# Kernel optimization log

Hardware: AMD Instinct MI355X
Metric: run time of the kernel (lower is better)

The kernel has to match this reference:

```python
import jax, jax.numpy as jnp
import numpy as np

B, S, D_MODEL = 1, 2048, 2048
H, KVH = 16, 4
HD = D_MODEL // H          # 128
N_REP = H // KVH           # 4 (GQA)
WINDOW = 1024              # window_size=(WINDOW-1, 0): self + 1023 past tokens
CLIP = 8.0
THETA = 500000.0
EPS = 1e-6
SCALE = 1.0 / (HD ** 0.5)


def rms_norm(x, w):
    # per-head RMSNorm over last dim (head_dim)
    var = jnp.mean(jnp.square(x), axis=-1, keepdims=True)
    return x * jax.lax.rsqrt(var + EPS) * w


def rope_tables():
    inv_freq = 1.0 / (THETA ** (jnp.arange(0, HD, 2, dtype=jnp.float32) / HD))
    pos = jnp.arange(S, dtype=jnp.float32)
    freqs = pos[:, None] * inv_freq[None, :]          # [S, HD/2]
    emb = jnp.concatenate([freqs, freqs], axis=-1)    # [S, HD]
    return jnp.cos(emb), jnp.sin(emb)


def rotate_half(x):
    x1, x2 = x[..., : HD // 2], x[..., HD // 2 :]
    return jnp.concatenate([-x2, x1], axis=-1)


def apply_rope(x, cos, sin):
    # x: [B, S, h, HD]; cos/sin: [S, HD]
    return x * cos[None, :, None, :] + rotate_half(x) * sin[None, :, None, :]


def setup_inputs() -> dict:
    key = jax.random.key(0)
    ks = jax.random.split(key, 7)
    w = lambda k, shape: jax.random.normal(k, shape, jnp.float32) * 0.02
    return {
        "x": jax.random.normal(ks[0], (B, S, D_MODEL), jnp.float32),
        "w_q": w(ks[1], (D_MODEL, D_MODEL)),
        "w_k": w(ks[2], (KVH * HD, D_MODEL)),
        "w_v": w(ks[3], (KVH * HD, D_MODEL)),
        "w_out": w(ks[4], (D_MODEL, D_MODEL)),
        "q_norm_w": jnp.ones((HD,), jnp.float32),
        "k_norm_w": jnp.ones((HD,), jnp.float32),
        "sinks": jax.random.normal(ks[5], (H,), jnp.float32),
    }


def reference(x, w_q, w_k, w_v, w_out, q_norm_w, k_norm_w, sinks):
    # fused QKV projection + clip
    q = jnp.clip(x @ w_q.T, -CLIP, CLIP).reshape(B, S, H, HD)
    k = jnp.clip(x @ w_k.T, -CLIP, CLIP).reshape(B, S, KVH, HD)
    v = jnp.clip(x @ w_v.T, -CLIP, CLIP).reshape(B, S, KVH, HD)

    # per-head qk RMSNorm, then RoPE
    q = rms_norm(q, q_norm_w)
    k = rms_norm(k, k_norm_w)
    cos, sin = rope_tables()
    q = apply_rope(q, cos, sin)
    k = apply_rope(k, cos, sin)

    # GQA: repeat_interleave kv heads
    k = jnp.repeat(k, N_REP, axis=2)  # [B, S, H, HD]
    v = jnp.repeat(v, N_REP, axis=2)

    # sliding-window causal attention with a learned per-head sink logit
    logits = jnp.einsum("bqhd,bkhd->bhqk", q, k) * SCALE  # [B, H, S, S]
    qi = jnp.arange(S)[:, None]
    ki = jnp.arange(S)[None, :]
    mask = (ki <= qi) & (ki > qi - WINDOW)                # causal + window
    logits = jnp.where(mask[None, None, :, :], logits, -jnp.inf)

    # sink token: always-visible extra logit sinks[h] with zero value vector
    sink_col = jnp.broadcast_to(sinks[None, :, None, None], (B, H, S, 1))
    full = jnp.concatenate([logits, sink_col], axis=-1)   # [B, H, S, S+1]
    probs = jax.nn.softmax(full, axis=-1)

    att = jnp.einsum("bhqk,bkhd->bqhd", probs[..., :S], v)  # sink value is 0
    return att.reshape(B, S, D_MODEL) @ w_out.T
```

## Files before the change

### kernel.cpp

```cpp
#include <hip/hip_runtime.h>
#include <hip/hip_bf16.h>
#include <math.h>

#define S_LEN 2048
#define DMODEL 2048
#define NH 16
#define NKVH 4
#define HDIM 128
#define WINDOW 1024

typedef __bf16 bf16;
typedef __bf16 bf16x8 __attribute__((ext_vector_type(8)));
typedef __bf16 bf16x4 __attribute__((ext_vector_type(4)));
typedef float floatx4 __attribute__((ext_vector_type(4)));

static __device__ __forceinline__ bf16x8 load_bf8(const bf16* p) {
    return *reinterpret_cast<const bf16x8*>(p);
}

static __device__ __forceinline__ void async16(const bf16* g, bf16* l) {
    __builtin_amdgcn_global_load_lds(
        (const __attribute__((address_space(1))) void*)g,
        (__attribute__((address_space(3))) void*)l, 16, 0, 0);
}

__global__ __launch_bounds__(256) void convert_kernel(
    const float* __restrict__ x, const float* __restrict__ wq,
    const float* __restrict__ wk, const float* __restrict__ wv,
    const float* __restrict__ wo,
    bf16* __restrict__ xb, bf16* __restrict__ wqb, bf16* __restrict__ wkb,
    bf16* __restrict__ wvb, bf16* __restrict__ wob) {
    for (int i = blockIdx.x * blockDim.x + threadIdx.x; i < 3670016;
         i += gridDim.x * blockDim.x) {
        const float* src; bf16* dst; int off;
        if      (i < 1048576) { src = x;  dst = xb;  off = i; }
        else if (i < 2097152) { src = wq; dst = wqb; off = i - 1048576; }
        else if (i < 2359296) { src = wk; dst = wkb; off = i - 2097152; }
        else if (i < 2621440) { src = wv; dst = wvb; off = i - 2359296; }
        else                  { src = wo; dst = wob; off = i - 2621440; }
        float4 v = reinterpret_cast<const float4*>(src)[off];
        union { bf16 b[4]; ushort4 u; } t;
        t.b[0] = (bf16)v.x; t.b[1] = (bf16)v.y;
        t.b[2] = (bf16)v.z; t.b[3] = (bf16)v.w;
        reinterpret_cast<ushort4*>(dst)[off] = t.u;
    }
}

__global__ __launch_bounds__(256, 1) void gemm_qkv_fused(
    const bf16* __restrict__ A, const bf16* __restrict__ B,
    const float* __restrict__ qw, const float* __restrict__ kw,
    bf16* __restrict__ qb, bf16* __restrict__ kb, bf16* __restrict__ vtb) {
    const int K = 2048;
    int flat = blockIdx.x;
    int xcd = flat & 7, w = flat >> 3;
    int mrow = xcd * 2 + (w >= 12);
    int ncol = (w >= 12) ? (w - 12) : w;
    int m0 = mrow * 128, n0 = ncol * 256;
    __shared__ __align__(16) bf16 smem[3 * 24576];
    int tid = threadIdx.x;
    int lane = tid & 63, wid = tid >> 6;
    int l15 = lane & 15, quad = lane >> 4;
    int rlocal = lane >> 3;
    int scol = ((lane & 7) ^ rlocal) * 8;
    const bf16* gA = A + (size_t)(m0 + wid * 32 + rlocal) * K + scol;
    const bf16* gB = B + (size_t)(n0 + wid * 64 + rlocal) * K + scol;
    int mb = (wid & 1) * 64, nb = (wid >> 1) * 128;

    floatx4 acc[4][8];
#pragma unroll
    for (int mi = 0; mi < 4; ++mi)
#pragma unroll
        for (int ni = 0; ni < 8; ++ni) acc[mi][ni] = floatx4{0.f, 0.f, 0.f, 0.f};

#pragma unroll
    for (int s = 0; s < 2; ++s) {
        bf16* dst = smem + s * 24576;
#pragma unroll
        for (int j = 0; j < 4; ++j)
            async16(gA + (size_t)(j * 8) * K + s * 64,
                    dst + (wid * 32 + j * 8) * 64);
#pragma unroll
        for (int j = 0; j < 8; ++j)
            async16(gB + (size_t)(j * 8) * K + s * 64,
                    dst + 8192 + (wid * 64 + j * 8) * 64);
    }

    int slot = 0;
#pragma unroll 1
    for (int t = 0; t < 32; ++t) {
        if (t < 31) asm volatile("s_waitcnt vmcnt(12)" ::: "memory");
        else        asm volatile("s_waitcnt vmcnt(0)" ::: "memory");
        __builtin_amdgcn_s_barrier();
        __builtin_amdgcn_sched_barrier(0);
        if (t < 30) {
            int s2 = slot + 2; if (s2 >= 3) s2 -= 3;
            bf16* dst = smem + s2 * 24576;
            int kof = (t + 2) * 64;
#pragma unroll
            for (int j = 0; j < 4; ++j)
                async16(gA + (size_t)(j * 8) * K + kof,
                        dst + (wid * 32 + j * 8) * 64);
#pragma unroll
            for (int j = 0; j < 8; ++j)
                async16(gB + (size_t)(j * 8) * K + kof,
                        dst + 8192 + (wid * 64 + j * 8) * 64);
        }
        const bf16* sA = smem + slot * 24576;
        const bf16* sB = sA + 8192;
#pragma unroll
        for (int kc = 0; kc < 2; ++kc) {
            bf16x8 af[4], bq[8];
            int ch = ((kc << 2) + quad) ^ (l15 & 7);
#pragma unroll
            for (int i = 0; i < 4; ++i)
                af[i] = load_bf8(sA + (mb + i * 16 + l15) * 64 + ch * 8);
#pragma unroll
            for (int n = 0; n < 8; ++n)
                bq[n] = load_bf8(sB + (nb + n * 16 + l15) * 64 + ch * 8);
#pragma unroll
            for (int mi = 0; mi < 4; ++mi)
#pragma unroll
                for (int ni = 0; ni < 8; ++ni)
                    acc[mi][ni] = __builtin_amdgcn_mfma_f32_16x16x32_bf16(
                        af[mi], bq[ni], acc[mi][ni], 0, 0, 0);
        }
        ++slot; if (slot == 3) slot = 0;
    }

#pragma unroll
    for (int mi = 0; mi < 4; ++mi)
#pragma unroll
        for (int ni = 0; ni < 8; ++ni)
#pragma unroll
            for (int r = 0; r < 4; ++r)
                acc[mi][ni][r] = fminf(fmaxf(acc[mi][ni][r], -8.0f), 8.0f);

    if (n0 >= 2560) {
#pragma unroll
        for (int mi = 0; mi < 4; ++mi)
#pragma unroll
            for (int ni = 0; ni < 8; ++ni)
#pragma unroll
                for (int r = 0; r < 4; ++r) {
                    int row = m0 + mb + mi * 16 + quad * 4 + r;
                    int n = n0 + nb + ni * 16 + l15;
                    vtb[(size_t)(n - 2560) * 2048 + row] = (bf16)acc[mi][ni][r];
                }
        return;
    }

    const float* nw = (n0 < 2048) ? qw : kw;
    float nwv[8];
#pragma unroll
    for (int ni = 0; ni < 8; ++ni) nwv[ni] = nw[(nb + ni * 16 + l15) & 127];
#pragma unroll
    for (int mi = 0; mi < 4; ++mi)
#pragma unroll
        for (int r = 0; r < 4; ++r) {
            float s = 0.f;
#pragma unroll
            for (int ni = 0; ni < 8; ++ni) s += acc[mi][ni][r] * acc[mi][ni][r];
#pragma unroll
            for (int o = 1; o < 16; o <<= 1) s += __shfl_xor(s, o, 64);
            float rinv = rsqrtf(s * (1.0f / 128.0f) + 1e-6f);
#pragma unroll
            for (int ni = 0; ni < 8; ++ni) acc[mi][ni][r] *= rinv * nwv[ni];
        }

    float invf[4];
#pragma unroll
    for (int ni = 0; ni < 4; ++ni) {
        int fi = ni * 16 + l15;
        invf[ni] = __expf((float)fi * (-13.122363377404328f / 64.0f));
    }
#pragma unroll
    for (int mi = 0; mi < 4; ++mi)
#pragma unroll
        for (int r = 0; r < 4; ++r) {
            int row = mb + mi * 16 + quad * 4 + r;
            int s = m0 + row;
            float pos = (float)s;
#pragma unroll
            for (int ni = 0; ni < 4; ++ni) {
                float ang = pos * invf[ni];
                float c = __cosf(ang), sn = __sinf(ang);
                float a = acc[mi][ni][r], b2 = acc[mi][ni + 4][r];
                float olo = a * c - b2 * sn;
                float ohi = b2 * c + a * sn;
                int nlo = n0 + nb + ni * 16 + l15;
                if (n0 < 2048) {
                    qb[(size_t)s * 2048 + nlo] = (bf16)olo;
                    qb[(size_t)s * 2048 + nlo + 64] = (bf16)ohi;
                } else {
                    kb[(size_t)s * 512 + (nlo - 2048)] = (bf16)olo;
                    kb[(size_t)s * 512 + (nlo - 2048) + 64] = (bf16)ohi;
                }
            }
        }
}

__global__ __launch_bounds__(256, 1) void gemm_out(
    const bf16* __restrict__ A, const bf16* __restrict__ B,
    float* __restrict__ C) {
    const int K = 2048, N = 2048;
    int flat = blockIdx.x;
    int xcd = flat & 7, w = flat >> 3;
    int m0 = (xcd * 2 + (w >> 4)) * 128;
    int n0 = (w & 15) * 128;
    __shared__ __align__(16) bf16 smem[3 * 16384];
    int tid = threadIdx.x;
    int lane = tid & 63, wid = tid >> 6;
    int l15 = lane & 15, quad = lane >> 4;
    int rlocal = lane >> 3;
    int scol = ((lane & 7) ^ rlocal) * 8;
    const bf16* gA = A + (size_t)(m0 + wid * 32 + rlocal) * K + scol;
    const bf16* gB = B + (size_t)(n0 + wid * 32 + rlocal) * K + scol;
    int mb = (wid & 1) * 64, nb = (wid >> 1) * 64;

    floatx4 acc[4][4];
#pragma unroll
    for (int mi = 0; mi < 4; ++mi)
#pragma unroll
        for (int ni = 0; ni < 4; ++ni) acc[mi][ni] = floatx4{0.f, 0.f, 0.f, 0.f};

#pragma unroll
    for (int s = 0; s < 2; ++s) {
        bf16* dst = smem + s * 16384;
#pragma unroll
        for (int j = 0; j < 4; ++j) {
            async16(gA + (size_t)(j * 8) * K + s * 64,
                    dst + (wid * 32 + j * 8) * 64);
            async16(gB + (size_t)(j * 8) * K + s * 64,
                    dst + 8192 + (wid * 32 + j * 8) * 64);
        }
    }

    int slot = 0;
#pragma unroll 1
    for (int t = 0; t < 32; ++t) {
        if (t < 31) asm volatile("s_waitcnt vmcnt(8)" ::: "memory");
        else        asm volatile("s_waitcnt vmcnt(0)" ::: "memory");
        __builtin_amdgcn_s_barrier();
        __builtin_amdgcn_sched_barrier(0);
        if (t < 30) {
            int s2 = slot + 2; if (s2 >= 3) s2 -= 3;
            bf16* dst = smem + s2 * 16384;
            int kof = (t + 2) * 64;
#pragma unroll
            for (int j = 0; j < 4; ++j) {
                async16(gA + (size_t)(j * 8) * K + kof,
                        dst + (wid * 32 + j * 8) * 64);
                async16(gB + (size_t)(j * 8) * K + kof,
                        dst + 8192 + (wid * 32 + j * 8) * 64);
            }
        }
        const bf16* sA = smem + slot * 16384;
        const bf16* sB = sA + 8192;
#pragma unroll
        for (int kc = 0; kc < 2; ++kc) {
            bf16x8 af[4], bq[4];
            int ch = ((kc << 2) + quad) ^ (l15 & 7);
#pragma unroll
            for (int i = 0; i < 4; ++i)
                af[i] = load_bf8(sA + (mb + i * 16 + l15) * 64 + ch * 8);
#pragma unroll
            for (int n = 0; n < 4; ++n)
                bq[n] = load_bf8(sB + (nb + n * 16 + l15) * 64 + ch * 8);
#pragma unroll
            for (int mi = 0; mi < 4; ++mi)
#pragma unroll
                for (int ni = 0; ni < 4; ++ni)
                    acc[mi][ni] = __builtin_amdgcn_mfma_f32_16x16x32_bf16(
                        af[mi], bq[ni], acc[mi][ni], 0, 0, 0);
        }
        ++slot; if (slot == 3) slot = 0;
    }

#pragma unroll
    for (int mi = 0; mi < 4; ++mi)
#pragma unroll
        for (int ni = 0; ni < 4; ++ni)
#pragma unroll
            for (int r = 0; r < 4; ++r) {
                int m = m0 + mb + mi * 16 + quad * 4 + r;
                int n = n0 + nb + ni * 16 + l15;
                C[(size_t)m * N + n] = acc[mi][ni][r];
            }
}

__global__ __launch_bounds__(256) void attn(
    const bf16* __restrict__ qb, const bf16* __restrict__ kb,
    const bf16* __restrict__ vtb, const float* __restrict__ sinks,
    bf16* __restrict__ attb) {
    __shared__ __align__(16) bf16 sK[2][64 * 128];
    __shared__ __align__(16) bf16 sV[2][128 * 64];
    __shared__ __align__(16) bf16 sP[64 * 72];
    __shared__ float redu[64][4];
    int tid = threadIdx.x;
    int lane = tid & 63, wid = tid >> 6;
    int l15 = lane & 15, quad = lane >> 4;
    int flat = blockIdx.x;
    int xcd = flat & 7, w = flat >> 3;
    int h = xcd * 2 + (w >> 5);
    int kh = h >> 2;
    int bq0 = (w & 31) * 64;

    bf16x8 qf[4][4];
#pragma unroll
    for (int ni = 0; ni < 4; ++ni) {
        const bf16* qrow = qb + (size_t)(bq0 + ni * 16 + l15) * 2048 + h * 128 + quad * 8;
#pragma unroll
        for (int kc = 0; kc < 4; ++kc) qf[ni][kc] = load_bf8(qrow + kc * 32);
    }

    floatx4 acc[4][2];
#pragma unroll
    for (int mi = 0; mi < 4; ++mi)
#pragma unroll
        for (int df = 0; df < 2; ++df) acc[mi][df] = floatx4{0.f, 0.f, 0.f, 0.f};
    float lpq[4];
#pragma unroll
    for (int ni = 0; ni < 4; ++ni) lpq[ni] = 0.f;

    int keyit = wid * 4 + (lane >> 4);
    int gcK = (lane & 15) ^ keyit;
    int dimit = wid * 8 + (lane >> 3);
    int gcV = (lane & 7) ^ ((lane >> 3) & 7);

    int tstart = bq0 - 1024; if (tstart < 0) tstart = 0;
    const bf16* kbase = kb + (size_t)kh * 128;
    const bf16* vbase = vtb + (size_t)kh * 128 * 2048;

#pragma unroll
    for (int r = 0; r < 4; ++r) {
        async16(kbase + (size_t)(tstart + r * 16 + keyit) * 512 + gcK * 8,
                sK[0] + (r * 16 + wid * 4) * 128);
        async16(vbase + (size_t)(r * 32 + dimit) * 2048 + tstart + gcV * 8,
                sV[0] + (r * 32 + wid * 8) * 64);
    }

    int buf = 0;
    for (int t = tstart; t <= bq0; t += 64) {
        __syncthreads();
        if (t + 64 <= bq0) {
#pragma unroll
            for (int r = 0; r < 4; ++r) {
                async16(kbase + (size_t)(t + 64 + r * 16 + keyit) * 512 + gcK * 8,
                        sK[buf ^ 1] + (r * 16 + wid * 4) * 128);
                async16(vbase + (size_t)(r * 32 + dimit) * 2048 + t + 64 + gcV * 8,
                        sV[buf ^ 1] + (r * 32 + wid * 8) * 64);
            }
        }
        floatx4 ST[4];
#pragma unroll
        for (int ni = 0; ni < 4; ++ni) ST[ni] = floatx4{0.f, 0.f, 0.f, 0.f};
#pragma unroll
        for (int kc = 0; kc < 4; ++kc) {
            int ch = (kc * 4 + quad) ^ l15;
            bf16x8 kf = load_bf8(sK[buf] + (wid * 16 + l15) * 128 + ch * 8);
#pragma unroll
            for (int ni = 0; ni < 4; ++ni)
                ST[ni] = __builtin_amdgcn_mfma_f32_16x16x32_bf16(kf, qf[ni][kc], ST[ni], 0, 0, 0);
        }
        int kbi = t + wid * 16 + quad * 4;
#pragma unroll
        for (int ni = 0; ni < 4; ++ni) {
            int qi = bq0 + ni * 16 + l15;
            bf16x4 pv;
#pragma unroll
            for (int r = 0; r < 4; ++r) {
                int ki = kbi + r;
                float v = ST[ni][r] * 0.08838834764831845f;
                bool ok = (ki <= qi) && (ki > qi - WINDOW);
                float e = ok ? __expf(v) : 0.0f;
                lpq[ni] += e;
                pv[r] = (bf16)e;
            }
            *(bf16x4*)(sP + (ni * 16 + l15) * 72 + wid * 16 + quad * 4) = pv;
        }
        __syncthreads();
#pragma unroll
        for (int kc = 0; kc < 2; ++kc) {
            bf16x8 pf[4];
#pragma unroll
            for (int mi = 0; mi < 4; ++mi)
                pf[mi] = load_bf8(sP + (mi * 16 + l15) * 72 + kc * 32 + quad * 8);
#pragma unroll
            for (int df = 0; df < 2; ++df) {
                int dim = wid * 32 + df * 16 + l15;
                int ch = (kc * 4 + quad) ^ (l15 & 7);
                bf16x8 vf = load_bf8(sV[buf] + dim * 64 + ch * 8);
#pragma unroll
                for (int mi = 0; mi < 4; ++mi)
                    acc[mi][df] = __builtin_amdgcn_mfma_f32_16x16x32_bf16(pf[mi], vf, acc[mi][df], 0, 0, 0);
            }
        }
        buf ^= 1;
    }

#pragma unroll
    for (int ni = 0; ni < 4; ++ni) {
        float v = lpq[ni];
        v += __shfl_xor(v, 16, 64);
        v += __shfl_xor(v, 32, 64);
        if (quad == 0) redu[ni * 16 + l15][wid] = v;
    }
    __syncthreads();
    float sk = __expf(sinks[h]);
#pragma unroll
    for (int mi = 0; mi < 4; ++mi)
#pragma unroll
        for (int r = 0; r < 4; ++r) {
            int row = mi * 16 + quad * 4 + r;
            float rs = redu[row][0] + redu[row][1] + redu[row][2] + redu[row][3] + sk;
            float inv = 1.0f / rs;
#pragma unroll
            for (int df = 0; df < 2; ++df) {
                int dim = wid * 32 + df * 16 + l15;
                attb[(size_t)(bq0 + row) * 2048 + h * 128 + dim] =
                    (bf16)(acc[mi][df][r] * inv);
            }
        }
}

extern "C" void kernel_launch(void* const* d_in, const int* in_sizes, int n_in,
                              void* d_out, int out_size, void* d_ws, size_t ws_size,
                              hipStream_t stream) {
    const float* x      = (const float*)d_in[0];
    const float* w_q    = (const float*)d_in[1];
    const float* w_k    = (const float*)d_in[2];
    const float* w_v    = (const float*)d_in[3];
    const float* w_out  = (const float*)d_in[4];
    const float* q_norm = (const float*)d_in[5];
    const float* k_norm = (const float*)d_in[6];
    const float* sinks  = (const float*)d_in[7];

    char* ws = (char*)d_ws;
    const size_t MB = 1u << 20;
    bf16* xb   = (bf16*)(ws + 0 * MB);
    bf16* wqb  = (bf16*)(ws + 8 * MB);
    bf16* wkb  = (bf16*)(ws + 16 * MB);
    bf16* wvb  = (bf16*)(ws + 18 * MB);
    bf16* wob  = (bf16*)(ws + 20 * MB);
    bf16* qb   = (bf16*)(ws + 28 * MB);
    bf16* kb   = (bf16*)(ws + 36 * MB);
    bf16* vtb  = (bf16*)(ws + 38 * MB);
    bf16* attb = (bf16*)(ws + 40 * MB);
    bf16* wcomb = wqb;
    float* out = (float*)d_out;

    convert_kernel<<<2048, 256, 0, stream>>>(x, w_q, w_k, w_v, w_out,
                                             xb, wqb, wkb, wvb, wob);
    gemm_qkv_fused<<<192, 256, 0, stream>>>(xb, wcomb, q_norm, k_norm,
                                            qb, kb, vtb);
    attn<<<512, 256, 0, stream>>>(qb, kb, vtb, sinks, attb);
    gemm_out<<<256, 256, 0, stream>>>(attb, wob, out);
}
```

Before: 205.1 us.

## Process 128 queries per attention block with 8 waves sharing K/V tiles

The attention kernel now uses 512-thread blocks that each cover 128 query rows (two 64-row halves), so every K/V tile staged in LDS serves twice as many queries. Staging is split so waves 0-3 load K and waves 4-7 load V, and the key loop runs one extra tile to cover the second query half. The intent is to halve global K/V traffic per query and the async loads per wave. In exchange the grid drops from 512 to 256 blocks, the XCD-aware block-to-head mapping is removed, and the first query half does useless masked work on its last tile.

```diff
diff --git a/kernel.cpp b/kernel.cpp
--- a/kernel.cpp
+++ b/kernel.cpp
@@ -288,27 +288,27 @@
             }
 }
 
-__global__ __launch_bounds__(256) void attn(
+__global__ __launch_bounds__(512) void attn(
     const bf16* __restrict__ qb, const bf16* __restrict__ kb,
     const bf16* __restrict__ vtb, const float* __restrict__ sinks,
     bf16* __restrict__ attb) {
     __shared__ __align__(16) bf16 sK[2][64 * 128];
     __shared__ __align__(16) bf16 sV[2][128 * 64];
-    __shared__ __align__(16) bf16 sP[64 * 72];
-    __shared__ float redu[64][4];
+    __shared__ __align__(16) bf16 sP[128 * 72];
+    __shared__ float redu[128][4];
     int tid = threadIdx.x;
     int lane = tid & 63, wid = tid >> 6;
     int l15 = lane & 15, quad = lane >> 4;
-    int flat = blockIdx.x;
-    int xcd = flat & 7, w = flat >> 3;
-    int h = xcd * 2 + (w >> 5);
-    int kh = h >> 2;
-    int bq0 = (w & 31) * 64;
+    int kq = wid >> 1;
+    int qh = wid & 1;
+    int h = blockIdx.y, kh = h >> 2;
+    int bq0 = blockIdx.x * 128;
 
     bf16x8 qf[4][4];
 #pragma unroll
     for (int ni = 0; ni < 4; ++ni) {
-        const bf16* qrow = qb + (size_t)(bq0 + ni * 16 + l15) * 2048 + h * 128 + quad * 8;
+        const bf16* qrow = qb + (size_t)(bq0 + qh * 64 + ni * 16 + l15) * 2048
+                           + h * 128 + quad * 8;
 #pragma unroll
         for (int kc = 0; kc < 4; ++kc) qf[ni][kc] = load_bf8(qrow + kc * 32);
     }
@@ -322,33 +322,44 @@
 #pragma unroll
     for (int ni = 0; ni < 4; ++ni) lpq[ni] = 0.f;
 
-    int keyit = wid * 4 + (lane >> 4);
+    int sw = wid & 3;
+    int keyit = sw * 4 + (lane >> 4);
     int gcK = (lane & 15) ^ keyit;
-    int dimit = wid * 8 + (lane >> 3);
+    int dimit = sw * 8 + (lane >> 3);
     int gcV = (lane & 7) ^ ((lane >> 3) & 7);
+    bool stageK = (wid < 4);
 
     int tstart = bq0 - 1024; if (tstart < 0) tstart = 0;
+    int tEnd = bq0 + 64;
     const bf16* kbase = kb + (size_t)kh * 128;
     const bf16* vbase = vtb + (size_t)kh * 128 * 2048;
 
-#pragma unroll
-    for (int r = 0; r < 4; ++r) {
-        async16(kbase + (size_t)(tstart + r * 16 + keyit) * 512 + gcK * 8,
-                sK[0] + (r * 16 + wid * 4) * 128);
-        async16(vbase + (size_t)(r * 32 + dimit) * 2048 + tstart + gcV * 8,
-                sV[0] + (r * 32 + wid * 8) * 64);
+    if (stageK) {
+#pragma unroll
+        for (int r = 0; r < 4; ++r)
+            async16(kbase + (size_t)(tstart + r * 16 + keyit) * 512 + gcK * 8,
+                    sK[0] + (r * 16 + sw * 4) * 128);
+    } else {
+#pragma unroll
+        for (int r = 0; r < 4; ++r)
+            async16(vbase + (size_t)(r * 32 + dimit) * 2048 + tstart + gcV * 8,
+                    sV[0] + (r * 32 + sw * 8) * 64);
     }
 
     int buf = 0;
-    for (int t = tstart; t <= bq0; t += 64) {
+    for (int t = tstart; t <= tEnd; t += 64) {
         __syncthreads();
-        if (t + 64 <= bq0) {
-#pragma unroll
-            for (int r = 0; r < 4; ++r) {
-                async16(kbase + (size_t)(t + 64 + r * 16 + keyit) * 512 + gcK * 8,
-                        sK[buf ^ 1] + (r * 16 + wid * 4) * 128);
-                async16(vbase + (size_t)(r * 32 + dimit) * 2048 + t + 64 + gcV * 8,
-                        sV[buf ^ 1] + (r * 32 + wid * 8) * 64);
+        if (t + 64 <= tEnd) {
+            if (stageK) {
+#pragma unroll
+                for (int r = 0; r < 4; ++r)
+                    async16(kbase + (size_t)(t + 64 + r * 16 + keyit) * 512 + gcK * 8,
+                            sK[buf ^ 1] + (r * 16 + sw * 4) * 128);
+            } else {
+#pragma unroll
+                for (int r = 0; r < 4; ++r)
+                    async16(vbase + (size_t)(r * 32 + dimit) * 2048 + t + 64 + gcV * 8,
+                            sV[buf ^ 1] + (r * 32 + sw * 8) * 64);
             }
         }
         floatx4 ST[4];
@@ -357,15 +368,15 @@
 #pragma unroll
         for (int kc = 0; kc < 4; ++kc) {
             int ch = (kc * 4 + quad) ^ l15;
-            bf16x8 kf = load_bf8(sK[buf] + (wid * 16 + l15) * 128 + ch * 8);
+            bf16x8 kf = load_bf8(sK[buf] + (kq * 16 + l15) * 128 + ch * 8);
 #pragma unroll
             for (int ni = 0; ni < 4; ++ni)
                 ST[ni] = __builtin_amdgcn_mfma_f32_16x16x32_bf16(kf, qf[ni][kc], ST[ni], 0, 0, 0);
         }
-        int kbi = t + wid * 16 + quad * 4;
+        int kbi = t + kq * 16 + quad * 4;
 #pragma unroll
         for (int ni = 0; ni < 4; ++ni) {
-            int qi = bq0 + ni * 16 + l15;
+            int qi = bq0 + qh * 64 + ni * 16 + l15;
             bf16x4 pv;
 #pragma unroll
             for (int r = 0; r < 4; ++r) {
@@ -376,7 +387,7 @@
                 lpq[ni] += e;
                 pv[r] = (bf16)e;
             }
-            *(bf16x4*)(sP + (ni * 16 + l15) * 72 + wid * 16 + quad * 4) = pv;
+            *(bf16x4*)(sP + (qh * 64 + ni * 16 + l15) * 72 + kq * 16 + quad * 4) = pv;
         }
         __syncthreads();
 #pragma unroll
@@ -384,10 +395,10 @@
             bf16x8 pf[4];
 #pragma unroll
             for (int mi = 0; mi < 4; ++mi)
-                pf[mi] = load_bf8(sP + (mi * 16 + l15) * 72 + kc * 32 + quad * 8);
+                pf[mi] = load_bf8(sP + (qh * 64 + mi * 16 + l15) * 72 + kc * 32 + quad * 8);
 #pragma unroll
             for (int df = 0; df < 2; ++df) {
-                int dim = wid * 32 + df * 16 + l15;
+                int dim = kq * 32 + df * 16 + l15;
                 int ch = (kc * 4 + quad) ^ (l15 & 7);
                 bf16x8 vf = load_bf8(sV[buf] + dim * 64 + ch * 8);
 #pragma unroll
@@ -403,7 +414,7 @@
         float v = lpq[ni];
         v += __shfl_xor(v, 16, 64);
         v += __shfl_xor(v, 32, 64);
-        if (quad == 0) redu[ni * 16 + l15][wid] = v;
+        if (quad == 0) redu[qh * 64 + ni * 16 + l15][kq] = v;
     }
     __syncthreads();
     float sk = __expf(sinks[h]);
@@ -411,12 +422,12 @@
     for (int mi = 0; mi < 4; ++mi)
 #pragma unroll
         for (int r = 0; r < 4; ++r) {
-            int row = mi * 16 + quad * 4 + r;
+            int row = qh * 64 + mi * 16 + quad * 4 + r;
             float rs = redu[row][0] + redu[row][1] + redu[row][2] + redu[row][3] + sk;
             float inv = 1.0f / rs;
 #pragma unroll
             for (int df = 0; df < 2; ++df) {
-                int dim = wid * 32 + df * 16 + l15;
+                int dim = kq * 32 + df * 16 + l15;
                 attb[(size_t)(bq0 + row) * 2048 + h * 128 + dim] =
                     (bf16)(acc[mi][df][r] * inv);
             }
@@ -453,6 +464,6 @@
                                              xb, wqb, wkb, wvb, wob);
     gemm_qkv_fused<<<192, 256, 0, stream>>>(xb, wcomb, q_norm, k_norm,
                                             qb, kb, vtb);
-    attn<<<512, 256, 0, stream>>>(qb, kb, vtb, sinks, attb);
+    attn<<<dim3(16, 16), 512, 0, stream>>>(qb, kb, vtb, sinks, attb);
     gemm_out<<<256, 256, 0, stream>>>(attb, wob, out);
 }
```

After: 206.5 us. About the same (+0.7%).

## Fuse all four stages into one persistent kernel with grid barriers

Applied to the files above, without the earlier changes.

Merges the convert, QKV GEMM, attention and output GEMM kernels into a single persistent kernel of 256 blocks, separated by atomic-counter grid barriers and sharing one 96KB shared-memory buffer. The aim is to remove the launch gaps and tail effects between kernels. In exchange, the GEMM pipelines drop from a triple-buffered pipeline with fine-grained vmcnt waits to plain double buffering. Attention now runs two units per block sequentially instead of 512 independent blocks. The one-block-per-CU launch bound plus spin barriers can lower occupancy, and the barriers rely on every block being co-resident.

```diff
diff --git a/kernel.cpp b/kernel.cpp
--- a/kernel.cpp
+++ b/kernel.cpp
@@ -2,11 +2,6 @@
 #include <hip/hip_bf16.h>
 #include <math.h>
 
-#define S_LEN 2048
-#define DMODEL 2048
-#define NH 16
-#define NKVH 4
-#define HDIM 128
 #define WINDOW 1024
 
 typedef __bf16 bf16;
@@ -24,14 +19,33 @@
         (__attribute__((address_space(3))) void*)l, 16, 0, 0);
 }
 
-__global__ __launch_bounds__(256) void convert_kernel(
+static __device__ __forceinline__ void gridbar(unsigned* ctr) {
+    __threadfence();
+    __syncthreads();
+    if (threadIdx.x == 0) {
+        atomicAdd(ctr, 1u);
+        while (atomicAdd(ctr, 0u) < 256u) __builtin_amdgcn_s_sleep(8);
+    }
+    __syncthreads();
+    __threadfence();
+}
+
+__global__ __launch_bounds__(256, 1) void fused_all(
     const float* __restrict__ x, const float* __restrict__ wq,
     const float* __restrict__ wk, const float* __restrict__ wv,
-    const float* __restrict__ wo,
+    const float* __restrict__ wo, const float* __restrict__ qnw,
+    const float* __restrict__ knw, const float* __restrict__ sinks,
     bf16* __restrict__ xb, bf16* __restrict__ wqb, bf16* __restrict__ wkb,
-    bf16* __restrict__ wvb, bf16* __restrict__ wob) {
-    for (int i = blockIdx.x * blockDim.x + threadIdx.x; i < 3670016;
-         i += gridDim.x * blockDim.x) {
+    bf16* __restrict__ wvb, bf16* __restrict__ wob, bf16* __restrict__ qb,
+    bf16* __restrict__ kb, bf16* __restrict__ vtb, bf16* __restrict__ attb,
+    float* __restrict__ out, unsigned* __restrict__ bar) {
+    __shared__ __align__(16) char sraw[98304];
+    int bid = blockIdx.x;
+    int tid = threadIdx.x;
+    int lane = tid & 63, wid = tid >> 6;
+    int l15 = lane & 15, quad = lane >> 4;
+
+    for (int i = bid * 256 + tid; i < 3670016; i += 256 * 256) {
         const float* src; bf16* dst; int off;
         if      (i < 1048576) { src = x;  dst = xb;  off = i; }
         else if (i < 2097152) { src = wq; dst = wqb; off = i - 1048576; }
@@ -44,383 +58,363 @@
         t.b[2] = (bf16)v.z; t.b[3] = (bf16)v.w;
         reinterpret_cast<ushort4*>(dst)[off] = t.u;
     }
-}
-
-__global__ __launch_bounds__(256, 1) void gemm_qkv_fused(
-    const bf16* __restrict__ A, const bf16* __restrict__ B,
-    const float* __restrict__ qw, const float* __restrict__ kw,
-    bf16* __restrict__ qb, bf16* __restrict__ kb, bf16* __restrict__ vtb) {
-    const int K = 2048;
-    int flat = blockIdx.x;
-    int xcd = flat & 7, w = flat >> 3;
-    int mrow = xcd * 2 + (w >= 12);
-    int ncol = (w >= 12) ? (w - 12) : w;
-    int m0 = mrow * 128, n0 = ncol * 256;
-    __shared__ __align__(16) bf16 smem[3 * 24576];
-    int tid = threadIdx.x;
-    int lane = tid & 63, wid = tid >> 6;
-    int l15 = lane & 15, quad = lane >> 4;
-    int rlocal = lane >> 3;
-    int scol = ((lane & 7) ^ rlocal) * 8;
-    const bf16* gA = A + (size_t)(m0 + wid * 32 + rlocal) * K + scol;
-    const bf16* gB = B + (size_t)(n0 + wid * 64 + rlocal) * K + scol;
-    int mb = (wid & 1) * 64, nb = (wid >> 1) * 128;
-
-    floatx4 acc[4][8];
-#pragma unroll
-    for (int mi = 0; mi < 4; ++mi)
-#pragma unroll
-        for (int ni = 0; ni < 8; ++ni) acc[mi][ni] = floatx4{0.f, 0.f, 0.f, 0.f};
-
-#pragma unroll
-    for (int s = 0; s < 2; ++s) {
-        bf16* dst = smem + s * 24576;
+    gridbar(bar + 0);
+
+    if (bid < 192) {
+        const int K = 2048;
+        int xcd = bid & 7, w = bid >> 3;
+        int mrow = xcd * 2 + (w >= 12);
+        int ncol = (w >= 12) ? (w - 12) : w;
+        int m0 = mrow * 128, n0 = ncol * 256;
+        bf16* smem = (bf16*)sraw;
+        const bf16* Bw = wqb;
+        int rlocal = lane >> 3;
+        int scol = ((lane & 7) ^ rlocal) * 8;
+        const bf16* gA = xb + (size_t)(m0 + wid * 32 + rlocal) * K + scol;
+        const bf16* gB = Bw + (size_t)(n0 + wid * 64 + rlocal) * K + scol;
+        int mb = (wid & 1) * 64, nb = (wid >> 1) * 128;
+
+        floatx4 acc[4][8];
+#pragma unroll
+        for (int mi = 0; mi < 4; ++mi)
+#pragma unroll
+            for (int ni = 0; ni < 8; ++ni)
+                acc[mi][ni] = floatx4{0.f, 0.f, 0.f, 0.f};
+
 #pragma unroll
         for (int j = 0; j < 4; ++j)
-            async16(gA + (size_t)(j * 8) * K + s * 64,
-                    dst + (wid * 32 + j * 8) * 64);
+            async16(gA + (size_t)(j * 8) * K, smem + (wid * 32 + j * 8) * 64);
 #pragma unroll
         for (int j = 0; j < 8; ++j)
-            async16(gB + (size_t)(j * 8) * K + s * 64,
-                    dst + 8192 + (wid * 64 + j * 8) * 64);
-    }
-
-    int slot = 0;
-#pragma unroll 1
-    for (int t = 0; t < 32; ++t) {
-        if (t < 31) asm volatile("s_waitcnt vmcnt(12)" ::: "memory");
-        else        asm volatile("s_waitcnt vmcnt(0)" ::: "memory");
-        __builtin_amdgcn_s_barrier();
-        __builtin_amdgcn_sched_barrier(0);
-        if (t < 30) {
-            int s2 = slot + 2; if (s2 >= 3) s2 -= 3;
-            bf16* dst = smem + s2 * 24576;
-            int kof = (t + 2) * 64;
-#pragma unroll
-            for (int j = 0; j < 4; ++j)
-                async16(gA + (size_t)(j * 8) * K + kof,
-                        dst + (wid * 32 + j * 8) * 64);
-#pragma unroll
-            for (int j = 0; j < 8; ++j)
-                async16(gB + (size_t)(j * 8) * K + kof,
-                        dst + 8192 + (wid * 64 + j * 8) * 64);
+            async16(gB + (size_t)(j * 8) * K,
+                    smem + 8192 + (wid * 64 + j * 8) * 64);
+
+        int buf = 0;
+        for (int k0 = 0; k0 < K; k0 += 64) {
+            __syncthreads();
+            if (k0 + 64 < K) {
+                bf16* nbase = smem + (buf ^ 1) * 24576;
+#pragma unroll
+                for (int j = 0; j < 4; ++j)
+                    async16(gA + (size_t)(j * 8) * K + k0 + 64,
+                            nbase + (wid * 32 + j * 8) * 64);
+#pragma unroll
+                for (int j = 0; j < 8; ++j)
+                    async16(gB + (size_t)(j * 8) * K + k0 + 64,
+                            nbase + 8192 + (wid * 64 + j * 8) * 64);
+            }
+            const bf16* sA = smem + buf * 24576;
+            const bf16* sB = sA + 8192;
+#pragma unroll
+            for (int kc = 0; kc < 2; ++kc) {
+                bf16x8 af[4], bq[8];
+                int ch = ((kc << 2) + quad) ^ (l15 & 7);
+#pragma unroll
+                for (int i = 0; i < 4; ++i)
+                    af[i] = load_bf8(sA + (mb + i * 16 + l15) * 64 + ch * 8);
+#pragma unroll
+                for (int n = 0; n < 8; ++n)
+                    bq[n] = load_bf8(sB + (nb + n * 16 + l15) * 64 + ch * 8);
+#pragma unroll
+                for (int mi = 0; mi < 4; ++mi)
+#pragma unroll
+                    for (int ni = 0; ni < 8; ++ni)
+                        acc[mi][ni] = __builtin_amdgcn_mfma_f32_16x16x32_bf16(
+                            af[mi], bq[ni], acc[mi][ni], 0, 0, 0);
+            }
+            buf ^= 1;
         }
-        const bf16* sA = smem + slot * 24576;
-        const bf16* sB = sA + 8192;
-#pragma unroll
-        for (int kc = 0; kc < 2; ++kc) {
-            bf16x8 af[4], bq[8];
-            int ch = ((kc << 2) + quad) ^ (l15 & 7);
-#pragma unroll
-            for (int i = 0; i < 4; ++i)
-                af[i] = load_bf8(sA + (mb + i * 16 + l15) * 64 + ch * 8);
-#pragma unroll
-            for (int n = 0; n < 8; ++n)
-                bq[n] = load_bf8(sB + (nb + n * 16 + l15) * 64 + ch * 8);
+
+#pragma unroll
+        for (int mi = 0; mi < 4; ++mi)
+#pragma unroll
+            for (int ni = 0; ni < 8; ++ni)
+#pragma unroll
+                for (int r = 0; r < 4; ++r)
+                    acc[mi][ni][r] = fminf(fmaxf(acc[mi][ni][r], -8.0f), 8.0f);
+
+        if (n0 >= 2560) {
 #pragma unroll
             for (int mi = 0; mi < 4; ++mi)
 #pragma unroll
                 for (int ni = 0; ni < 8; ++ni)
-                    acc[mi][ni] = __builtin_amdgcn_mfma_f32_16x16x32_bf16(
-                        af[mi], bq[ni], acc[mi][ni], 0, 0, 0);
-        }
-        ++slot; if (slot == 3) slot = 0;
-    }
-
-#pragma unroll
-    for (int mi = 0; mi < 4; ++mi)
-#pragma unroll
-        for (int ni = 0; ni < 8; ++ni)
-#pragma unroll
-            for (int r = 0; r < 4; ++r)
-                acc[mi][ni][r] = fminf(fmaxf(acc[mi][ni][r], -8.0f), 8.0f);
-
-    if (n0 >= 2560) {
-#pragma unroll
-        for (int mi = 0; mi < 4; ++mi)
+#pragma unroll
+                    for (int r = 0; r < 4; ++r) {
+                        int row = m0 + mb + mi * 16 + quad * 4 + r;
+                        int n = n0 + nb + ni * 16 + l15;
+                        vtb[(size_t)(n - 2560) * 2048 + row] =
+                            (bf16)acc[mi][ni][r];
+                    }
+        } else {
+            const float* nw = (n0 < 2048) ? qnw : knw;
+            float nwv[8];
 #pragma unroll
             for (int ni = 0; ni < 8; ++ni)
+                nwv[ni] = nw[(nb + ni * 16 + l15) & 127];
+#pragma unroll
+            for (int mi = 0; mi < 4; ++mi)
 #pragma unroll
                 for (int r = 0; r < 4; ++r) {
-                    int row = m0 + mb + mi * 16 + quad * 4 + r;
-                    int n = n0 + nb + ni * 16 + l15;
-                    vtb[(size_t)(n - 2560) * 2048 + row] = (bf16)acc[mi][ni][r];
-                }
-        return;
-    }
-
-    const float* nw = (n0 < 2048) ? qw : kw;
-    float nwv[8];
-#pragma unroll
-    for (int ni = 0; ni < 8; ++ni) nwv[ni] = nw[(nb + ni * 16 + l15) & 127];
-#pragma unroll
-    for (int mi = 0; mi < 4; ++mi)
-#pragma unroll
-        for (int r = 0; r < 4; ++r) {
-            float s = 0.f;
-#pragma unroll
-            for (int ni = 0; ni < 8; ++ni) s += acc[mi][ni][r] * acc[mi][ni][r];
-#pragma unroll
-            for (int o = 1; o < 16; o <<= 1) s += __shfl_xor(s, o, 64);
-            float rinv = rsqrtf(s * (1.0f / 128.0f) + 1e-6f);
-#pragma unroll
-            for (int ni = 0; ni < 8; ++ni) acc[mi][ni][r] *= rinv * nwv[ni];
-        }
-
-    float invf[4];
-#pragma unroll
-    for (int ni = 0; ni < 4; ++ni) {
-        int fi = ni * 16 + l15;
-        invf[ni] = __expf((float)fi * (-13.122363377404328f / 64.0f));
-    }
-#pragma unroll
-    for (int mi = 0; mi < 4; ++mi)
-#pragma unroll
-        for (int r = 0; r < 4; ++r) {
-            int row = mb + mi * 16 + quad * 4 + r;
-            int s = m0 + row;
-            float pos = (float)s;
+                    float s = 0.f;
+#pragma unroll
+                    for (int ni = 0; ni < 8; ++ni)
+                        s += acc[mi][ni][r] * acc[mi][ni][r];
+#pragma unroll
+                    for (int o = 1; o < 16; o <<= 1) s += __shfl_xor(s, o, 64);
+                    float rinv = rsqrtf(s * (1.0f / 128.0f) + 1e-6f);
+#pragma unroll
+                    for (int ni = 0; ni < 8; ++ni)
+                        acc[mi][ni][r] *= rinv * nwv[ni];
+                }
+            float invf[4];
 #pragma unroll
             for (int ni = 0; ni < 4; ++ni) {
-                float ang = pos * invf[ni];
-                float c = __cosf(ang), sn = __sinf(ang);
-                float a = acc[mi][ni][r], b2 = acc[mi][ni + 4][r];
-                float olo = a * c - b2 * sn;
-                float ohi = b2 * c + a * sn;
-                int nlo = n0 + nb + ni * 16 + l15;
-                if (n0 < 2048) {
-                    qb[(size_t)s * 2048 + nlo] = (bf16)olo;
-                    qb[(size_t)s * 2048 + nlo + 64] = (bf16)ohi;
-                } else {
-                    kb[(size_t)s * 512 + (nlo - 2048)] = (bf16)olo;
-                    kb[(size_t)s * 512 + (nlo - 2048) + 64] = (bf16)ohi;
-                }
-            }
-        }
-}
-
-__global__ __launch_bounds__(256, 1) void gemm_out(
-    const bf16* __restrict__ A, const bf16* __restrict__ B,
-    float* __restrict__ C) {
-    const int K = 2048, N = 2048;
-    int flat = blockIdx.x;
-    int xcd = flat & 7, w = flat >> 3;
-    int m0 = (xcd * 2 + (w >> 4)) * 128;
-    int n0 = (w & 15) * 128;
-    __shared__ __align__(16) bf16 smem[3 * 16384];
-    int tid = threadIdx.x;
-    int lane = tid & 63, wid = tid >> 6;
-    int l15 = lane & 15, quad = lane >> 4;
-    int rlocal = lane >> 3;
-    int scol = ((lane & 7) ^ rlocal) * 8;
-    const bf16* gA = A + (size_t)(m0 + wid * 32 + rlocal) * K + scol;
-    const bf16* gB = B + (size_t)(n0 + wid * 32 + rlocal) * K + scol;
-    int mb = (wid & 1) * 64, nb = (wid >> 1) * 64;
-
-    floatx4 acc[4][4];
-#pragma unroll
-    for (int mi = 0; mi < 4; ++mi)
-#pragma unroll
-        for (int ni = 0; ni < 4; ++ni) acc[mi][ni] = floatx4{0.f, 0.f, 0.f, 0.f};
-
-#pragma unroll
-    for (int s = 0; s < 2; ++s) {
-        bf16* dst = smem + s * 16384;
-#pragma unroll
-        for (int j = 0; j < 4; ++j) {
-            async16(gA + (size_t)(j * 8) * K + s * 64,
-                    dst + (wid * 32 + j * 8) * 64);
-            async16(gB + (size_t)(j * 8) * K + s * 64,
-                    dst + 8192 + (wid * 32 + j * 8) * 64);
+                int fi = ni * 16 + l15;
+                invf[ni] = __expf((float)fi * (-13.122363377404328f / 64.0f));
+            }
+#pragma unroll
+            for (int mi = 0; mi < 4; ++mi)
+#pragma unroll
+                for (int r = 0; r < 4; ++r) {
+                    int row = mb + mi * 16 + quad * 4 + r;
+                    int s = m0 + row;
+                    float pos = (float)s;
+#pragma unroll
+                    for (int ni = 0; ni < 4; ++ni) {
+                        float ang = pos * invf[ni];
+                        float c = __cosf(ang), sn = __sinf(ang);
+                        float a = acc[mi][ni][r], b2 = acc[mi][ni + 4][r];
+                        float olo = a * c - b2 * sn;
+                        float ohi = b2 * c + a * sn;
+                        int nlo = n0 + nb + ni * 16 + l15;
+                        if (n0 < 2048) {
+                            qb[(size_t)s * 2048 + nlo] = (bf16)olo;
+                            qb[(size_t)s * 2048 + nlo + 64] = (bf16)ohi;
+                        } else {
+                            kb[(size_t)s * 512 + (nlo - 2048)] = (bf16)olo;
+                            kb[(size_t)s * 512 + (nlo - 2048) + 64] = (bf16)ohi;
+                        }
+                    }
+                }
         }
     }
-
-    int slot = 0;
-#pragma unroll 1
-    for (int t = 0; t < 32; ++t) {
-        if (t < 31) asm volatile("s_waitcnt vmcnt(8)" ::: "memory");
-        else        asm volatile("s_waitcnt vmcnt(0)" ::: "memory");
-        __builtin_amdgcn_s_barrier();
-        __builtin_amdgcn_sched_barrier(0);
-        if (t < 30) {
-            int s2 = slot + 2; if (s2 >= 3) s2 -= 3;
-            bf16* dst = smem + s2 * 16384;
-            int kof = (t + 2) * 64;
-#pragma unroll
-            for (int j = 0; j < 4; ++j) {
-                async16(gA + (size_t)(j * 8) * K + kof,
-                        dst + (wid * 32 + j * 8) * 64);
-                async16(gB + (size_t)(j * 8) * K + kof,
-                        dst + 8192 + (wid * 32 + j * 8) * 64);
-            }
+    gridbar(bar + 1);
+
+    {
+        bf16* sK0 = (bf16*)sraw;
+        bf16* sV0 = (bf16*)(sraw + 32768);
+        bf16* sP  = (bf16*)(sraw + 65536);
+        float (*redu)[4] = (float(*)[4])(sraw + 65536 + 9216);
+
+        for (int u = 0; u < 2; ++u) {
+            int unit = bid * 2 + u;
+            int xcd = unit & 7, w = unit >> 3;
+            int h = xcd * 2 + (w >> 5);
+            int kh = h >> 2;
+            int bq0 = (w & 31) * 64;
+            __syncthreads();
+
+            bf16x8 qf[4][4];
+#pragma unroll
+            for (int ni = 0; ni < 4; ++ni) {
+                const bf16* qrow = qb + (size_t)(bq0 + ni * 16 + l15) * 2048 +
+                                   h * 128 + quad * 8;
+#pragma unroll
+                for (int kc = 0; kc < 4; ++kc)
+                    qf[ni][kc] = load_bf8(qrow + kc * 32);
+            }
+
+            floatx4 acc[4][2];
+#pragma unroll
+            for (int mi = 0; mi < 4; ++mi)
+#pragma unroll
+                for (int df = 0; df < 2; ++df)
+                    acc[mi][df] = floatx4{0.f, 0.f, 0.f, 0.f};
+            float lpq[4];
+#pragma unroll
+            for (int ni = 0; ni < 4; ++ni) lpq[ni] = 0.f;
+
+            int keyit = wid * 4 + (lane >> 4);
+            int gcK = (lane & 15) ^ keyit;
+            int dimit = wid * 8 + (lane >> 3);
+            int gcV = (lane & 7) ^ ((lane >> 3) & 7);
+
+            int tstart = bq0 - 1024; if (tstart < 0) tstart = 0;
+            const bf16* kbase = kb + (size_t)kh * 128;
+            const bf16* vbase = vtb + (size_t)kh * 128 * 2048;
+
+#pragma unroll
+            for (int r = 0; r < 4; ++r) {
+                async16(kbase + (size_t)(tstart + r * 16 + keyit) * 512 + gcK * 8,
+                        sK0 + (r * 16 + wid * 4) * 128);
+                async16(vbase + (size_t)(r * 32 + dimit) * 2048 + tstart + gcV * 8,
+                        sV0 + (r * 32 + wid * 8) * 64);
+            }
+
+            int buf = 0;
+            for (int t = tstart; t <= bq0; t += 64) {
+                __syncthreads();
+                if (t + 64 <= bq0) {
+#pragma unroll
+                    for (int r = 0; r < 4; ++r) {
+                        async16(kbase + (size_t)(t + 64 + r * 16 + keyit) * 512 + gcK * 8,
+                                sK0 + (buf ^ 1) * 8192 + (r * 16 + wid * 4) * 128);
+                        async16(vbase + (size_t)(r * 32 + dimit) * 2048 + t + 64 + gcV * 8,
+                                sV0 + (buf ^ 1) * 8192 + (r * 32 + wid * 8) * 64);
+                    }
+                }
+                floatx4 ST[4];
+#pragma unroll
+                for (int ni = 0; ni < 4; ++ni)
+                    ST[ni] = floatx4{0.f, 0.f, 0.f, 0.f};
+#pragma unroll
+                for (int kc = 0; kc < 4; ++kc) {
+                    int ch = (kc * 4 + quad) ^ l15;
+                    bf16x8 kf = load_bf8(sK0 + buf * 8192 +
+                                         (wid * 16 + l15) * 128 + ch * 8);
+#pragma unroll
+                    for (int ni = 0; ni < 4; ++ni)
+                        ST[ni] = __builtin_amdgcn_mfma_f32_16x16x32_bf16(
+                            kf, qf[ni][kc], ST[ni], 0, 0, 0);
+                }
+                int kbi = t + wid * 16 + quad * 4;
+#pragma unroll
+                for (int ni = 0; ni < 4; ++ni) {
+                    int qi = bq0 + ni * 16 + l15;
+                    bf16x4 pv;
+#pragma unroll
+                    for (int r = 0; r < 4; ++r) {
+                        int ki = kbi + r;
+                        float v = ST[ni][r] * 0.08838834764831845f;
+                        bool ok = (ki <= qi) && (ki > qi - WINDOW);
+                        float e = ok ? __expf(v) : 0.0f;
+                        lpq[ni] += e;
+                        pv[r] = (bf16)e;
+                    }
+                    *(bf16x4*)(sP + (ni * 16 + l15) * 72 + wid * 16 + quad * 4) = pv;
+                }
+                __syncthreads();
+#pragma unroll
+                for (int kc = 0; kc < 2; ++kc) {
+                    bf16x8 pf[4];
+#pragma unroll
+                    for (int mi = 0; mi < 4; ++mi)
+                        pf[mi] = load_bf8(sP + (mi * 16 + l15) * 72 +
+                                          kc * 32 + quad * 8);
+#pragma unroll
+                    for (int df = 0; df < 2; ++df) {
+                        int dim = wid * 32 + df * 16 + l15;
+                        int ch = (kc * 4 + quad) ^ (l15 & 7);
+                        bf16x8 vf = load_bf8(sV0 + buf * 8192 + dim * 64 + ch * 8);
+#pragma unroll
+                        for (int mi = 0; mi < 4; ++mi)
+                            acc[mi][df] = __builtin_amdgcn_mfma_f32_16x16x32_bf16(
+                                pf[mi], vf, acc[mi][df], 0, 0, 0);
+                    }
+                }
+                buf ^= 1;
+            }
+
+#pragma unroll
+            for (int ni = 0; ni < 4; ++ni) {
+                float v = lpq[ni];
+                v += __shfl_xor(v, 16, 64);
+                v += __shfl_xor(v, 32, 64);
+                if (quad == 0) redu[ni * 16 + l15][wid] = v;
+            }
+            __syncthreads();
+            float sk = __expf(sinks[h]);
+#pragma unroll
+            for (int mi = 0; mi < 4; ++mi)
+#pragma unroll
+                for (int r = 0; r < 4; ++r) {
+                    int row = mi * 16 + quad * 4 + r;
+                    float rs = redu[row][0] + redu[row][1] + redu[row][2] +
+                               redu[row][3] + sk;
+                    float inv = 1.0f / rs;
+#pragma unroll
+                    for (int df = 0; df < 2; ++df) {
+                        int dim = wid * 32 + df * 16 + l15;
+                        attb[(size_t)(bq0 + row) * 2048 + h * 128 + dim] =
+                            (bf16)(acc[mi][df][r] * inv);
+                    }
+                }
         }
-        const bf16* sA = smem + slot * 16384;
-        const bf16* sB = sA + 8192;
-#pragma unroll
-        for (int kc = 0; kc < 2; ++kc) {
-            bf16x8 af[4], bq[4];
-            int ch = ((kc << 2) + quad) ^ (l15 & 7);
-#pragma unroll
-            for (int i = 0; i < 4; ++i)
-                af[i] = load_bf8(sA + (mb + i * 16 + l15) * 64 + ch * 8);
-#pragma unroll
-            for (int n = 0; n < 4; ++n)
-                bq[n] = load_bf8(sB + (nb + n * 16 + l15) * 64 + ch * 8);
-#pragma unroll
-            for (int mi = 0; mi < 4; ++mi)
-#pragma unroll
-                for (int ni = 0; ni < 4; ++ni)
-                    acc[mi][ni] = __builtin_amdgcn_mfma_f32_16x16x32_bf16(
-                        af[mi], bq[ni], acc[mi][ni], 0, 0, 0);
+    }
+    gridbar(bar + 2);
+
+    {
+        const int K = 2048, N = 2048;
+        int xcd = bid & 7, w = bid >> 3;
+        int m0 = (xcd * 2 + (w >> 4)) * 128;
+        int n0 = (w & 15) * 128;
+        bf16* smem = (bf16*)sraw;
+        int rlocal = lane >> 3;
+        int scol = ((lane & 7) ^ rlocal) * 8;
+        const bf16* gA = attb + (size_t)(m0 + wid * 32 + rlocal) * K + scol;
+        const bf16* gB = wob + (size_t)(n0 + wid * 32 + rlocal) * K + scol;
+        int mb = (wid & 1) * 64, nb = (wid >> 1) * 64;
+
+        floatx4 acc[4][4];
+#pragma unroll
+        for (int mi = 0; mi < 4; ++mi)
+#pragma unroll
+            for (int ni = 0; ni < 4; ++ni)
+                acc[mi][ni] = floatx4{0.f, 0.f, 0.f, 0.f};
+
+#pragma unroll
+        for (int j = 0; j < 4; ++j) {
+            async16(gA + (size_t)(j * 8) * K, smem + (wid * 32 + j * 8) * 64);
+            async16(gB + (size_t)(j * 8) * K,
+                    smem + 8192 + (wid * 32 + j * 8) * 64);
         }
-        ++slot; if (slot == 3) slot = 0;
+
+        int buf = 0;
+        for (int k0 = 0; k0 < K; k0 += 64) {
+            __syncthreads();
+            if (k0 + 64 < K) {
+                bf16* nbase = smem + (buf ^ 1) * 16384;
+#pragma unroll
+                for (int j = 0; j < 4; ++j) {
+                    async16(gA + (size_t)(j * 8) * K + k0 + 64,
+                            nbase + (wid * 32 + j * 8) * 64);
+                    async16(gB + (size_t)(j * 8) * K + k0 + 64,
+                            nbase + 8192 + (wid * 32 + j * 8) * 64);
+                }
+            }
+            const bf16* sA = smem + buf * 16384;
+            const bf16* sB = sA + 8192;
+#pragma unroll
+            for (int kc = 0; kc < 2; ++kc) {
+                bf16x8 af[4], bq[4];
+                int ch = ((kc << 2) + quad) ^ (l15 & 7);
+#pragma unroll
+                for (int i = 0; i < 4; ++i)
+                    af[i] = load_bf8(sA + (mb + i * 16 + l15) * 64 + ch * 8);
+#pragma unroll
+                for (int n = 0; n < 4; ++n)
+                    bq[n] = load_bf8(sB + (nb + n * 16 + l15) * 64 + ch * 8);
+#pragma unroll
+                for (int mi = 0; mi < 4; ++mi)
+#pragma unroll
+                    for (int ni = 0; ni < 4; ++ni)
+                        acc[mi][ni] = __builtin_amdgcn_mfma_f32_16x16x32_bf16(
+                            af[mi], bq[ni], acc[mi][ni], 0, 0, 0);
+            }
+            buf ^= 1;
+        }
+
+#pragma unroll
+        for (int mi = 0; mi < 4; ++mi)
+#pragma unroll
+            for (int ni = 0; ni < 4; ++ni)
+#pragma unroll
+                for (int r = 0; r < 4; ++r) {
+                    int m = m0 + mb + mi * 16 + quad * 4 + r;
+                    int n = n0 + nb + ni * 16 + l15;
+                    out[(size_t)m * N + n] = acc[mi][ni][r];
+                }
     }
-
-#pragma unroll
-    for (int mi = 0; mi < 4; ++mi)
-#pragma unroll
-        for (int ni = 0; ni < 4; ++ni)
-#pragma unroll
-            for (int r = 0; r < 4; ++r) {
-                int m = m0 + mb + mi * 16 + quad * 4 + r;
-                int n = n0 + nb + ni * 16 + l15;
-                C[(size_t)m * N + n] = acc[mi][ni][r];
-            }
-}
-
-__global__ __launch_bounds__(256) void attn(
-    const bf16* __restrict__ qb, const bf16* __restrict__ kb,
-    const bf16* __restrict__ vtb, const float* __restrict__ sinks,
-    bf16* __restrict__ attb) {
-    __shared__ __align__(16) bf16 sK[2][64 * 128];
-    __shared__ __align__(16) bf16 sV[2][128 * 64];
-    __shared__ __align__(16) bf16 sP[64 * 72];
-    __shared__ float redu[64][4];
-    int tid = threadIdx.x;
-    int lane = tid & 63, wid = tid >> 6;
-    int l15 = lane & 15, quad = lane >> 4;
-    int flat = blockIdx.x;
-    int xcd = flat & 7, w = flat >> 3;
-    int h = xcd * 2 + (w >> 5);
-    int kh = h >> 2;
-    int bq0 = (w & 31) * 64;
-
-    bf16x8 qf[4][4];
-#pragma unroll
-    for (int ni = 0; ni < 4; ++ni) {
-        const bf16* qrow = qb + (size_t)(bq0 + ni * 16 + l15) * 2048 + h * 128 + quad * 8;
-#pragma unroll
-        for (int kc = 0; kc < 4; ++kc) qf[ni][kc] = load_bf8(qrow + kc * 32);
-    }
-
-    floatx4 acc[4][2];
-#pragma unroll
-    for (int mi = 0; mi < 4; ++mi)
-#pragma unroll
-        for (int df = 0; df < 2; ++df) acc[mi][df] = floatx4{0.f, 0.f, 0.f, 0.f};
-    float lpq[4];
-#pragma unroll
-    for (int ni = 0; ni < 4; ++ni) lpq[ni] = 0.f;
-
-    int keyit = wid * 4 + (lane >> 4);
-    int gcK = (lane & 15) ^ keyit;
-    int dimit = wid * 8 + (lane >> 3);
-    int gcV = (lane & 7) ^ ((lane >> 3) & 7);
-
-    int tstart = bq0 - 1024; if (tstart < 0) tstart = 0;
-    const bf16* kbase = kb + (size_t)kh * 128;
-    const bf16* vbase = vtb + (size_t)kh * 128 * 2048;
-
-#pragma unroll
-    for (int r = 0; r < 4; ++r) {
-        async16(kbase + (size_t)(tstart + r * 16 + keyit) * 512 + gcK * 8,
-                sK[0] + (r * 16 + wid * 4) * 128);
-        async16(vbase + (size_t)(r * 32 + dimit) * 2048 + tstart + gcV * 8,
-                sV[0] + (r * 32 + wid * 8) * 64);
-    }
-
-    int buf = 0;
-    for (int t = tstart; t <= bq0; t += 64) {
-        __syncthreads();
-        if (t + 64 <= bq0) {
-#pragma unroll
-            for (int r = 0; r < 4; ++r) {
-                async16(kbase + (size_t)(t + 64 + r * 16 + keyit) * 512 + gcK * 8,
-                        sK[buf ^ 1] + (r * 16 + wid * 4) * 128);
-                async16(vbase + (size_t)(r * 32 + dimit) * 2048 + t + 64 + gcV * 8,
-                        sV[buf ^ 1] + (r * 32 + wid * 8) * 64);
-            }
-        }
-        floatx4 ST[4];
-#pragma unroll
-        for (int ni = 0; ni < 4; ++ni) ST[ni] = floatx4{0.f, 0.f, 0.f, 0.f};
-#pragma unroll
-        for (int kc = 0; kc < 4; ++kc) {
-            int ch = (kc * 4 + quad) ^ l15;
-            bf16x8 kf = load_bf8(sK[buf] + (wid * 16 + l15) * 128 + ch * 8);
-#pragma unroll
-            for (int ni = 0; ni < 4; ++ni)
-                ST[ni] = __builtin_amdgcn_mfma_f32_16x16x32_bf16(kf, qf[ni][kc], ST[ni], 0, 0, 0);
-        }
-        int kbi = t + wid * 16 + quad * 4;
-#pragma unroll
-        for (int ni = 0; ni < 4; ++ni) {
-            int qi = bq0 + ni * 16 + l15;
-            bf16x4 pv;
-#pragma unroll
-            for (int r = 0; r < 4; ++r) {
-                int ki = kbi + r;
-                float v = ST[ni][r] * 0.08838834764831845f;
-                bool ok = (ki <= qi) && (ki > qi - WINDOW);
-                float e = ok ? __expf(v) : 0.0f;
-                lpq[ni] += e;
-                pv[r] = (bf16)e;
-            }
-            *(bf16x4*)(sP + (ni * 16 + l15) * 72 + wid * 16 + quad * 4) = pv;
-        }
-        __syncthreads();
-#pragma unroll
-        for (int kc = 0; kc < 2; ++kc) {
-            bf16x8 pf[4];
-#pragma unroll
-            for (int mi = 0; mi < 4; ++mi)
-                pf[mi] = load_bf8(sP + (mi * 16 + l15) * 72 + kc * 32 + quad * 8);
-#pragma unroll
-            for (int df = 0; df < 2; ++df) {
-                int dim = wid * 32 + df * 16 + l15;
-                int ch = (kc * 4 + quad) ^ (l15 & 7);
-                bf16x8 vf = load_bf8(sV[buf] + dim * 64 + ch * 8);
-#pragma unroll
-                for (int mi = 0; mi < 4; ++mi)
-                    acc[mi][df] = __builtin_amdgcn_mfma_f32_16x16x32_bf16(pf[mi], vf, acc[mi][df], 0, 0, 0);
-            }
-        }
-        buf ^= 1;
-    }
-
-#pragma unroll
-    for (int ni = 0; ni < 4; ++ni) {
-        float v = lpq[ni];
-        v += __shfl_xor(v, 16, 64);
-        v += __shfl_xor(v, 32, 64);
-        if (quad == 0) redu[ni * 16 + l15][wid] = v;
-    }
-    __syncthreads();
-    float sk = __expf(sinks[h]);
-#pragma unroll
-    for (int mi = 0; mi < 4; ++mi)
-#pragma unroll
-        for (int r = 0; r < 4; ++r) {
-            int row = mi * 16 + quad * 4 + r;
-            float rs = redu[row][0] + redu[row][1] + redu[row][2] + redu[row][3] + sk;
-            float inv = 1.0f / rs;
-#pragma unroll
-            for (int df = 0; df < 2; ++df) {
-                int dim = wid * 32 + df * 16 + l15;
-                attb[(size_t)(bq0 + row) * 2048 + h * 128 + dim] =
-                    (bf16)(acc[mi][df][r] * inv);
-            }
-        }
 }
 
 extern "C" void kernel_launch(void* const* d_in, const int* in_sizes, int n_in,
@@ -446,13 +440,11 @@
     bf16* kb   = (bf16*)(ws + 36 * MB);
     bf16* vtb  = (bf16*)(ws + 38 * MB);
     bf16* attb = (bf16*)(ws + 40 * MB);
-    bf16* wcomb = wqb;
+    unsigned* bar = (unsigned*)(ws + 48 * MB);
     float* out = (float*)d_out;
 
-    convert_kernel<<<2048, 256, 0, stream>>>(x, w_q, w_k, w_v, w_out,
-                                             xb, wqb, wkb, wvb, wob);
-    gemm_qkv_fused<<<192, 256, 0, stream>>>(xb, wcomb, q_norm, k_norm,
-                                            qb, kb, vtb);
-    attn<<<512, 256, 0, stream>>>(qb, kb, vtb, sinks, attb);
-    gemm_out<<<256, 256, 0, stream>>>(attb, wob, out);
+    hipMemsetAsync(bar, 0, 16, stream);
+    fused_all<<<256, 256, 0, stream>>>(
+        x, w_q, w_k, w_v, w_out, q_norm, k_norm, sinks,
+        xb, wqb, wkb, wvb, wob, qb, kb, vtb, attb, out, bar);
 }
```

After: 386.7 us. 1.89x slower.
